# Optimization experiments

Measured on AMD Instinct MI355X. Metric: run time of the kernel, lower is better.

Reference implementation:

```python
import jax, jax.numpy as jnp
import numpy as np

B, L, H, E, M = 4, 4096, 8, 64, 64
IN_CH, OUT_CH = 512, 512
SCALE = 1.0 / (IN_CH * OUT_CH)


def setup_inputs() -> dict:
    key = jax.random.key(0)
    k0, k1, k2, k3, k4 = jax.random.split(key, 5)
    q = jax.random.normal(k0, (B, L, H, E), dtype=jnp.float32)
    k = jax.random.normal(k1, (B, L, H, E), dtype=jnp.float32)
    v = jax.random.normal(k2, (B, L, H, E), dtype=jnp.float32)
    # torch.rand on a complex dtype fills real and imag parts with U[0,1)
    w_real = SCALE * jax.random.uniform(k3, (H, H, E, M), dtype=jnp.float32)
    w_imag = SCALE * jax.random.uniform(k4, (H, H, E, M), dtype=jnp.float32)
    # mode_select_method != 'random' -> lowest M modes, sorted
    index = jnp.arange(M, dtype=jnp.int32)
    mask = 0
    return {"q": q, "k": k, "v": v, "w_real": w_real, "w_imag": w_imag, "index": index, "mask": mask}


def reference(q, k, v, w_real, w_imag, index, mask):
    weights = w_real + 1j * w_imag                      # [H,H,E,M] complex64
    x = jnp.transpose(q, (0, 2, 3, 1))                   # [B,H,E,L]
    x_ft = jnp.fft.rfft(x, axis=-1)                      # [B,H,E,L//2+1]
    xg = jnp.take(x_ft, index, axis=-1)                  # gather selected modes: [B,H,E,M]
    # per-(E, mode) head-mixing: 'bix,iox->box' batched over modes
    res = jnp.einsum('bixm,ioxm->boxm', xg, weights)     # [B,H,E,M]
    Lh = L // 2 + 1
    out_ft = jnp.zeros((B, H, E, Lh), dtype=res.dtype).at[..., :M].set(res)
    x_out = jnp.fft.irfft(out_ft, n=L, axis=-1)          # [B,H,E,L] float32
    return x_out
```

## Files before the change

### kernel.cpp

```cpp
#include <hip/hip_runtime.h>

#define Bsz 4
#define Lsz 4096
#define HEsz 512
#define SPLIT 16

typedef __attribute__((ext_vector_type(8))) short short8;
typedef __attribute__((ext_vector_type(4))) float f32x4;

#define OFF_BASFT 0u
#define OFF_BASIT (1u<<20)
#define OFF_CF    (2u<<20)
#define OFF_C1P   (3u<<20)

static __device__ __forceinline__ unsigned short f2bf(float f) {
    union { float f; unsigned u; } v; v.f = f;
    unsigned u = v.u;
    return (unsigned short)((u + 0x7fffu + ((u >> 16) & 1u)) >> 16);
}
static __device__ __forceinline__ unsigned pk2(float a, float b) {
    return (unsigned)f2bf(a) | ((unsigned)f2bf(b) << 16);
}
static __device__ __forceinline__ void sc(int m, int l, float* s, float* c) {
    int r = (m * l) & (Lsz - 1);
    float ang = (float)r * (6.283185307179586f / (float)Lsz);
    __sincosf(ang, s, c);
}

__global__ __launch_bounds__(256) void k_tables(unsigned short* __restrict__ basFT,
                                                unsigned short* __restrict__ basIT) {
    int bid = blockIdx.x, t = threadIdx.x;
    if (bid < 256) {
        int tid = bid * 256 + t;
        int c = tid >> 9, lg = tid & 511;
        int m = c >> 1, im = c & 1;
        float v[8];
#pragma unroll
        for (int j = 0; j < 8; ++j) {
            float s, co; sc(m, lg * 8 + j, &s, &co);
            v[j] = im ? -s : co;
        }
        uint4 o = make_uint4(pk2(v[0], v[1]), pk2(v[2], v[3]), pk2(v[4], v[5]), pk2(v[6], v[7]));
        *(uint4*)(basFT + (size_t)c * Lsz + lg * 8) = o;
    } else {
        int tid = (bid - 256) * 256 + t;
        int l = tid >> 4, mg = tid & 15;
        unsigned w[4];
#pragma unroll
        for (int jm = 0; jm < 4; ++jm) {
            int m = mg * 4 + jm;
            float s, co; sc(m, l, &s, &co);
            float wm = (m == 0) ? (1.0f / Lsz) : (2.0f / Lsz);
            w[jm] = pk2(wm * co, wm * s);
        }
        *(uint4*)(basIT + (size_t)l * 128 + mg * 8) = make_uint4(w[0], w[1], w[2], w[3]);
    }
}

__global__ __launch_bounds__(256, 2) void k_dft(const float* __restrict__ q,
                                                const unsigned short* __restrict__ basFT,
                                                float* __restrict__ C1P) {
    __shared__ unsigned short As[64 * 64];
    __shared__ unsigned short Bs[128 * 64];
    const int ks = blockIdx.x, ht = blockIdx.y, b = blockIdx.z;
    const int he0 = ht * 64;
    const int t = threadIdx.x, lane = t & 63, w = t >> 6;
    const int wm = w & 1, wn = w >> 1;
    const int quad = lane >> 4, lid = lane & 15;
    f32x4 acc[2][4] = {};

    const int kbeg = ks * (Lsz / SPLIT);
    for (int ch = 0; ch < 4; ++ch) {
        const int l0 = kbeg + ch * 64;
        {
            const float* qp = q + ((size_t)(b * Lsz + l0 + w * 16) * HEsz + he0 + lane);
            float f[16];
#pragma unroll
            for (int j = 0; j < 16; ++j) f[j] = qp[(size_t)j * HEsz];
            uint4 p0 = make_uint4(pk2(f[0], f[1]), pk2(f[2], f[3]), pk2(f[4], f[5]), pk2(f[6], f[7]));
            uint4 p1 = make_uint4(pk2(f[8], f[9]), pk2(f[10], f[11]), pk2(f[12], f[13]), pk2(f[14], f[15]));
            int row = lane;
            int cb0 = (w * 2) ^ (row & 7), cb1 = (w * 2 + 1) ^ (row & 7);
            *(uint4*)(As + row * 64 + cb0 * 8) = p0;
            *(uint4*)(As + row * 64 + cb1 * 8) = p1;
        }
#pragma unroll
        for (int it = 0; it < 4; ++it) {
            int slot = t + it * 256;
            int c = slot >> 3, cb = slot & 7;
            uint4 v = *(const uint4*)(basFT + (size_t)c * Lsz + l0 + cb * 8);
            *(uint4*)(Bs + c * 64 + ((cb ^ (c & 7)) * 8)) = v;
        }
        __syncthreads();
#pragma unroll
        for (int kst = 0; kst < 2; ++kst) {
            short8 af[2], bfr[4];
#pragma unroll
            for (int mt = 0; mt < 2; ++mt) {
                int m = wm * 32 + mt * 16 + lid;
                int cb = (kst * 4 + quad) ^ (m & 7);
                af[mt] = *(short8*)(As + m * 64 + cb * 8);
            }
#pragma unroll
            for (int nt = 0; nt < 4; ++nt) {
                int n = wn * 64 + nt * 16 + lid;
                int cb = (kst * 4 + quad) ^ (n & 7);
                bfr[nt] = *(short8*)(Bs + n * 64 + cb * 8);
            }
#pragma unroll
            for (int mt = 0; mt < 2; ++mt)
#pragma unroll
                for (int nt = 0; nt < 4; ++nt)
                    acc[mt][nt] = __builtin_amdgcn_mfma_f32_16x16x32_bf16(af[mt], bfr[nt], acc[mt][nt], 0, 0, 0);
        }
        __syncthreads();
    }
    float* dst = C1P + (((size_t)ks * Bsz + b) * HEsz + he0) * 128;
#pragma unroll
    for (int mt = 0; mt < 2; ++mt)
#pragma unroll
        for (int nt = 0; nt < 4; ++nt)
#pragma unroll
            for (int r = 0; r < 4; ++r)
                dst[(size_t)(wm * 32 + mt * 16 + quad * 4 + r) * 128 + wn * 64 + nt * 16 + lid] =
                    acc[mt][nt][r];
}

__global__ __launch_bounds__(256) void k_mixreduce(const float* __restrict__ C1P,
                                                   const float* __restrict__ wr,
                                                   const float* __restrict__ wi,
                                                   unsigned short* __restrict__ Cf) {
    __shared__ float X[8][128];
    const int e = blockIdx.x & 63, b = blockIdx.x >> 6;
    const int t = threadIdx.x;
    const int i = t >> 5, c4 = t & 31;
    const float4* base = (const float4*)(C1P + (((size_t)b * HEsz + i * 64 + e) * 128)) + c4;
    float4 s = make_float4(0.f, 0.f, 0.f, 0.f);
    for (int sp = 0; sp < SPLIT; ++sp) {
        float4 v = base[(size_t)sp * (Bsz * HEsz * 128 / 4)];
        s.x += v.x; s.y += v.y; s.z += v.z; s.w += v.w;
    }
    *(float4*)&X[i][c4 * 4] = s;
    __syncthreads();
#pragma unroll
    for (int it = 0; it < 2; ++it) {
        int item = t + it * 256;
        int o = item >> 6, m = item & 63;
        float ar = 0.f, ai = 0.f;
#pragma unroll
        for (int i2 = 0; i2 < 8; ++i2) {
            float xr = X[i2][2 * m], xi = X[i2][2 * m + 1];
            size_t wo = ((size_t)(i2 * 8 + o) * 64 + e) * 64 + m;
            float wrv = wr[wo], wiv = wi[wo];
            ar += xr * wrv - xi * wiv;
            ai += xr * wiv + xi * wrv;
        }
        int row = b * HEsz + o * 64 + e;
        *(unsigned*)(Cf + (size_t)row * 128 + 2 * m) = pk2(ar, -ai);
    }
}

__global__ __launch_bounds__(256, 2) void k_idft(const unsigned short* __restrict__ Cf,
                                                 const unsigned short* __restrict__ basIT,
                                                 float* __restrict__ out) {
    __shared__ unsigned short As[128 * 128];
    __shared__ unsigned short Bs[128 * 128];
    const int l0 = blockIdx.x * 128, row0 = blockIdx.y * 128;
    const int t = threadIdx.x, lane = t & 63, w = t >> 6;
    const int wm = w & 1, wn = w >> 1;
    const int quad = lane >> 4, lid = lane & 15;
#pragma unroll
    for (int it = 0; it < 8; ++it) {
        int slot = t + it * 256;
        int r = slot >> 4, cb = slot & 15;
        uint4 a = *(const uint4*)(Cf + (size_t)(row0 + r) * 128 + cb * 8);
        *(uint4*)(As + r * 128 + ((cb ^ (r & 15)) * 8)) = a;
        uint4 bv = *(const uint4*)(basIT + (size_t)(l0 + r) * 128 + cb * 8);
        *(uint4*)(Bs + r * 128 + ((cb ^ (r & 15)) * 8)) = bv;
    }
    __syncthreads();
    f32x4 acc[4][4] = {};
#pragma unroll
    for (int kst = 0; kst < 4; ++kst) {
        short8 af[4], bfr[4];
#pragma unroll
        for (int mt = 0; mt < 4; ++mt) {
            int m = wm * 64 + mt * 16 + lid;
            int cb = (kst * 4 + quad) ^ (m & 15);
            af[mt] = *(short8*)(As + m * 128 + cb * 8);
        }
#pragma unroll
        for (int nt = 0; nt < 4; ++nt) {
            int n = wn * 64 + nt * 16 + lid;
            int cb = (kst * 4 + quad) ^ (n & 15);
            bfr[nt] = *(short8*)(Bs + n * 128 + cb * 8);
        }
#pragma unroll
        for (int mt = 0; mt < 4; ++mt)
#pragma unroll
            for (int nt = 0; nt < 4; ++nt)
                acc[mt][nt] = __builtin_amdgcn_mfma_f32_16x16x32_bf16(af[mt], bfr[nt], acc[mt][nt], 0, 0, 0);
    }
    __syncthreads();
    float* outb = (float*)As;
#pragma unroll
    for (int mt = 0; mt < 4; ++mt)
#pragma unroll
        for (int nt = 0; nt < 4; ++nt)
#pragma unroll
            for (int r = 0; r < 4; ++r)
                outb[(size_t)(wm * 64 + mt * 16 + quad * 4 + r) * 128 + wn * 64 + nt * 16 + lid] =
                    acc[mt][nt][r];
    __syncthreads();
#pragma unroll
    for (int it = 0; it < 16; ++it) {
        int slot = t + it * 256;
        int r = slot >> 5, c4 = slot & 31;
        float4 v = *(float4*)(outb + (size_t)r * 128 + c4 * 4);
        *(float4*)(out + (size_t)(row0 + r) * Lsz + l0 + c4 * 4) = v;
    }
}

extern "C" void kernel_launch(void* const* d_in, const int* in_sizes, int n_in,
                              void* d_out, int out_size, void* d_ws, size_t ws_size,
                              hipStream_t stream) {
    const float* q      = (const float*)d_in[0];
    const float* w_real = (const float*)d_in[3];
    const float* w_imag = (const float*)d_in[4];
    float* out = (float*)d_out;
    char* ws = (char*)d_ws;

    unsigned short* basFT = (unsigned short*)(ws + OFF_BASFT);
    unsigned short* basIT = (unsigned short*)(ws + OFF_BASIT);
    unsigned short* Cf    = (unsigned short*)(ws + OFF_CF);
    float*          C1P   = (float*)(ws + OFF_C1P);

    k_tables   <<<512, 256, 0, stream>>>(basFT, basIT);
    k_dft      <<<dim3(SPLIT, 8, 4), 256, 0, stream>>>(q, basFT, C1P);
    k_mixreduce<<<256, 256, 0, stream>>>(C1P, w_real, w_imag, Cf);
    k_idft     <<<dim3(32, 16), 256, 0, stream>>>(Cf, basIT, out);
}
```

Measured before the change: 146.8 us.

## Compute DFT twiddles inline in GEMM kernels and store partials in bf16

Removes the separate table-building kernel and computes the forward and inverse DFT basis values with sincos directly into shared memory inside k_dft and k_idft. This saves a launch and the global reads of the basis tables, at the cost of recomputing sincos in every block. The split-K partial sums are also stored as bf16 instead of fp32, which halves that intermediate traffic but adds rounding error before the reduction.

```diff
diff --git a/kernel.cpp b/kernel.cpp
--- a/kernel.cpp
+++ b/kernel.cpp
@@ -8,10 +8,8 @@
 typedef __attribute__((ext_vector_type(8))) short short8;
 typedef __attribute__((ext_vector_type(4))) float f32x4;
 
-#define OFF_BASFT 0u
-#define OFF_BASIT (1u<<20)
-#define OFF_CF    (2u<<20)
-#define OFF_C1P   (3u<<20)
+#define OFF_CF  0u
+#define OFF_C1P (1u<<20)
 
 static __device__ __forceinline__ unsigned short f2bf(float f) {
     union { float f; unsigned u; } v; v.f = f;
@@ -21,51 +19,24 @@
 static __device__ __forceinline__ unsigned pk2(float a, float b) {
     return (unsigned)f2bf(a) | ((unsigned)f2bf(b) << 16);
 }
+static __device__ __forceinline__ float bf2f(unsigned short u) {
+    union { unsigned u; float f; } v; v.u = ((unsigned)u) << 16;
+    return v.f;
+}
 static __device__ __forceinline__ void sc(int m, int l, float* s, float* c) {
     int r = (m * l) & (Lsz - 1);
     float ang = (float)r * (6.283185307179586f / (float)Lsz);
     __sincosf(ang, s, c);
 }
 
-__global__ __launch_bounds__(256) void k_tables(unsigned short* __restrict__ basFT,
-                                                unsigned short* __restrict__ basIT) {
-    int bid = blockIdx.x, t = threadIdx.x;
-    if (bid < 256) {
-        int tid = bid * 256 + t;
-        int c = tid >> 9, lg = tid & 511;
-        int m = c >> 1, im = c & 1;
-        float v[8];
-#pragma unroll
-        for (int j = 0; j < 8; ++j) {
-            float s, co; sc(m, lg * 8 + j, &s, &co);
-            v[j] = im ? -s : co;
-        }
-        uint4 o = make_uint4(pk2(v[0], v[1]), pk2(v[2], v[3]), pk2(v[4], v[5]), pk2(v[6], v[7]));
-        *(uint4*)(basFT + (size_t)c * Lsz + lg * 8) = o;
-    } else {
-        int tid = (bid - 256) * 256 + t;
-        int l = tid >> 4, mg = tid & 15;
-        unsigned w[4];
-#pragma unroll
-        for (int jm = 0; jm < 4; ++jm) {
-            int m = mg * 4 + jm;
-            float s, co; sc(m, l, &s, &co);
-            float wm = (m == 0) ? (1.0f / Lsz) : (2.0f / Lsz);
-            w[jm] = pk2(wm * co, wm * s);
-        }
-        *(uint4*)(basIT + (size_t)l * 128 + mg * 8) = make_uint4(w[0], w[1], w[2], w[3]);
-    }
-}
-
 __global__ __launch_bounds__(256, 2) void k_dft(const float* __restrict__ q,
-                                                const unsigned short* __restrict__ basFT,
-                                                float* __restrict__ C1P) {
+                                                unsigned short* __restrict__ C1P) {
     __shared__ unsigned short As[64 * 64];
     __shared__ unsigned short Bs[128 * 64];
     const int ks = blockIdx.x, ht = blockIdx.y, b = blockIdx.z;
     const int he0 = ht * 64;
     const int t = threadIdx.x, lane = t & 63, w = t >> 6;
-    const int wm = w & 1, wn = w >> 1;
+    const int wtm = w & 1, wtn = w >> 1;
     const int quad = lane >> 4, lid = lane & 15;
     f32x4 acc[2][4] = {};
 
@@ -84,12 +55,23 @@
             *(uint4*)(As + row * 64 + cb0 * 8) = p0;
             *(uint4*)(As + row * 64 + cb1 * 8) = p1;
         }
-#pragma unroll
-        for (int it = 0; it < 4; ++it) {
-            int slot = t + it * 256;
-            int c = slot >> 3, cb = slot & 7;
-            uint4 v = *(const uint4*)(basFT + (size_t)c * Lsz + l0 + cb * 8);
-            *(uint4*)(Bs + c * 64 + ((cb ^ (c & 7)) * 8)) = v;
+        {
+            int m = t & 63, lg = t >> 6;
+            int c0 = 2 * m, c1 = 2 * m + 1;
+#pragma unroll
+            for (int h = 0; h < 2; ++h) {
+                float sv[8], cv[8];
+#pragma unroll
+                for (int j = 0; j < 8; ++j)
+                    sc(m, l0 + lg * 16 + h * 8 + j, &sv[j], &cv[j]);
+                uint4 pc = make_uint4(pk2(cv[0], cv[1]), pk2(cv[2], cv[3]),
+                                      pk2(cv[4], cv[5]), pk2(cv[6], cv[7]));
+                uint4 ps = make_uint4(pk2(-sv[0], -sv[1]), pk2(-sv[2], -sv[3]),
+                                      pk2(-sv[4], -sv[5]), pk2(-sv[6], -sv[7]));
+                int lb = lg * 2 + h;
+                *(uint4*)(Bs + c0 * 64 + ((lb ^ (c0 & 7)) * 8)) = pc;
+                *(uint4*)(Bs + c1 * 64 + ((lb ^ (c1 & 7)) * 8)) = ps;
+            }
         }
         __syncthreads();
 #pragma unroll
@@ -97,13 +79,13 @@
             short8 af[2], bfr[4];
 #pragma unroll
             for (int mt = 0; mt < 2; ++mt) {
-                int m = wm * 32 + mt * 16 + lid;
+                int m = wtm * 32 + mt * 16 + lid;
                 int cb = (kst * 4 + quad) ^ (m & 7);
                 af[mt] = *(short8*)(As + m * 64 + cb * 8);
             }
 #pragma unroll
             for (int nt = 0; nt < 4; ++nt) {
-                int n = wn * 64 + nt * 16 + lid;
+                int n = wtn * 64 + nt * 16 + lid;
                 int cb = (kst * 4 + quad) ^ (n & 7);
                 bfr[nt] = *(short8*)(Bs + n * 64 + cb * 8);
             }
@@ -115,18 +97,18 @@
         }
         __syncthreads();
     }
-    float* dst = C1P + (((size_t)ks * Bsz + b) * HEsz + he0) * 128;
+    unsigned short* dst = C1P + (((size_t)ks * Bsz + b) * HEsz + he0) * 128;
 #pragma unroll
     for (int mt = 0; mt < 2; ++mt)
 #pragma unroll
         for (int nt = 0; nt < 4; ++nt)
 #pragma unroll
             for (int r = 0; r < 4; ++r)
-                dst[(size_t)(wm * 32 + mt * 16 + quad * 4 + r) * 128 + wn * 64 + nt * 16 + lid] =
-                    acc[mt][nt][r];
-}
-
-__global__ __launch_bounds__(256) void k_mixreduce(const float* __restrict__ C1P,
+                dst[(size_t)(wtm * 32 + mt * 16 + quad * 4 + r) * 128 + wtn * 64 + nt * 16 + lid] =
+                    f2bf(acc[mt][nt][r]);
+}
+
+__global__ __launch_bounds__(256) void k_mixreduce(const unsigned short* __restrict__ C1P,
                                                    const float* __restrict__ wr,
                                                    const float* __restrict__ wi,
                                                    unsigned short* __restrict__ Cf) {
@@ -134,13 +116,16 @@
     const int e = blockIdx.x & 63, b = blockIdx.x >> 6;
     const int t = threadIdx.x;
     const int i = t >> 5, c4 = t & 31;
-    const float4* base = (const float4*)(C1P + (((size_t)b * HEsz + i * 64 + e) * 128)) + c4;
-    float4 s = make_float4(0.f, 0.f, 0.f, 0.f);
+    size_t off = ((size_t)b * HEsz + i * 64 + e) * 128 + c4 * 4;
+    float sx = 0.f, sy = 0.f, sz = 0.f, sw = 0.f;
     for (int sp = 0; sp < SPLIT; ++sp) {
-        float4 v = base[(size_t)sp * (Bsz * HEsz * 128 / 4)];
-        s.x += v.x; s.y += v.y; s.z += v.z; s.w += v.w;
-    }
-    *(float4*)&X[i][c4 * 4] = s;
+        uint2 v = *(const uint2*)(C1P + off + (size_t)sp * (Bsz * HEsz * 128));
+        sx += bf2f((unsigned short)(v.x & 0xffff));
+        sy += bf2f((unsigned short)(v.x >> 16));
+        sz += bf2f((unsigned short)(v.y & 0xffff));
+        sw += bf2f((unsigned short)(v.y >> 16));
+    }
+    *(float4*)&X[i][c4 * 4] = make_float4(sx, sy, sz, sw);
     __syncthreads();
 #pragma unroll
     for (int it = 0; it < 2; ++it) {
@@ -161,13 +146,12 @@
 }
 
 __global__ __launch_bounds__(256, 2) void k_idft(const unsigned short* __restrict__ Cf,
-                                                 const unsigned short* __restrict__ basIT,
                                                  float* __restrict__ out) {
     __shared__ unsigned short As[128 * 128];
     __shared__ unsigned short Bs[128 * 128];
     const int l0 = blockIdx.x * 128, row0 = blockIdx.y * 128;
     const int t = threadIdx.x, lane = t & 63, w = t >> 6;
-    const int wm = w & 1, wn = w >> 1;
+    const int wtm = w & 1, wtn = w >> 1;
     const int quad = lane >> 4, lid = lane & 15;
 #pragma unroll
     for (int it = 0; it < 8; ++it) {
@@ -175,8 +159,24 @@
         int r = slot >> 4, cb = slot & 15;
         uint4 a = *(const uint4*)(Cf + (size_t)(row0 + r) * 128 + cb * 8);
         *(uint4*)(As + r * 128 + ((cb ^ (r & 15)) * 8)) = a;
-        uint4 bv = *(const uint4*)(basIT + (size_t)(l0 + r) * 128 + cb * 8);
-        *(uint4*)(Bs + r * 128 + ((cb ^ (r & 15)) * 8)) = bv;
+    }
+    {
+        int lr = t >> 1, half = t & 1;
+        int lg = l0 + lr;
+#pragma unroll
+        for (int jj = 0; jj < 8; ++jj) {
+            unsigned wv[4];
+#pragma unroll
+            for (int j = 0; j < 4; ++j) {
+                int m = half * 32 + jj * 4 + j;
+                float s, co; sc(m, lg, &s, &co);
+                float wm = (m == 0) ? (1.0f / Lsz) : (2.0f / Lsz);
+                wv[j] = pk2(wm * co, wm * s);
+            }
+            int cb = half * 8 + jj;
+            *(uint4*)(Bs + lr * 128 + ((cb ^ (lr & 15)) * 8)) =
+                make_uint4(wv[0], wv[1], wv[2], wv[3]);
+        }
     }
     __syncthreads();
     f32x4 acc[4][4] = {};
@@ -185,13 +185,13 @@
         short8 af[4], bfr[4];
 #pragma unroll
         for (int mt = 0; mt < 4; ++mt) {
-            int m = wm * 64 + mt * 16 + lid;
+            int m = wtm * 64 + mt * 16 + lid;
             int cb = (kst * 4 + quad) ^ (m & 15);
             af[mt] = *(short8*)(As + m * 128 + cb * 8);
         }
 #pragma unroll
         for (int nt = 0; nt < 4; ++nt) {
-            int n = wn * 64 + nt * 16 + lid;
+            int n = wtn * 64 + nt * 16 + lid;
             int cb = (kst * 4 + quad) ^ (n & 15);
             bfr[nt] = *(short8*)(Bs + n * 128 + cb * 8);
         }
@@ -209,7 +209,7 @@
         for (int nt = 0; nt < 4; ++nt)
 #pragma unroll
             for (int r = 0; r < 4; ++r)
-                outb[(size_t)(wm * 64 + mt * 16 + quad * 4 + r) * 128 + wn * 64 + nt * 16 + lid] =
+                outb[(size_t)(wtm * 64 + mt * 16 + quad * 4 + r) * 128 + wtn * 64 + nt * 16 + lid] =
                     acc[mt][nt][r];
     __syncthreads();
 #pragma unroll
@@ -230,13 +230,10 @@
     float* out = (float*)d_out;
     char* ws = (char*)d_ws;
 
-    unsigned short* basFT = (unsigned short*)(ws + OFF_BASFT);
-    unsigned short* basIT = (unsigned short*)(ws + OFF_BASIT);
-    unsigned short* Cf    = (unsigned short*)(ws + OFF_CF);
-    float*          C1P   = (float*)(ws + OFF_C1P);
-
-    k_tables   <<<512, 256, 0, stream>>>(basFT, basIT);
-    k_dft      <<<dim3(SPLIT, 8, 4), 256, 0, stream>>>(q, basFT, C1P);
+    unsigned short* Cf  = (unsigned short*)(ws + OFF_CF);
+    unsigned short* C1P = (unsigned short*)(ws + OFF_C1P);
+
+    k_dft      <<<dim3(SPLIT, 8, 4), 256, 0, stream>>>(q, C1P);
     k_mixreduce<<<256, 256, 0, stream>>>(C1P, w_real, w_imag, Cf);
-    k_idft     <<<dim3(32, 16), 256, 0, stream>>>(Cf, basIT, out);
-}
+    k_idft     <<<dim3(32, 16), 256, 0, stream>>>(Cf, out);
+}
```

New measurement: 145.1 us. Within noise of the previous version (-1.2%).
